# Kernel optimization log

Hardware: AMD Instinct MI355X
Metric: run time of the kernel (lower is better)

The kernel has to match this reference:

```python
import jax, jax.numpy as jnp
import numpy as np

NEG = -1e30


def setup_inputs() -> dict:
    key = jax.random.key(0)
    ks = jax.random.split(key, 8)
    B, d, Lc, Lq = 32, 128, 2048, 512
    C = jax.random.normal(ks[0], (B, d, Lc), dtype=jnp.float32)
    Q = jax.random.normal(ks[1], (B, d, Lq), dtype=jnp.float32)
    Cmask = jax.random.randint(ks[2], (B, Lc), 0, 2, dtype=jnp.int32)
    Qmask = jax.random.randint(ks[3], (B, Lq), 0, 2, dtype=jnp.int32)
    # xavier_uniform over (d, 1): bound = sqrt(6 / (d + 1))
    bnd = float(np.sqrt(6.0 / (d + 1)))
    w_c = jax.random.uniform(ks[4], (d, 1), minval=-bnd, maxval=bnd, dtype=jnp.float32)
    w_q = jax.random.uniform(ks[5], (d, 1), minval=-bnd, maxval=bnd, dtype=jnp.float32)
    bnd_m = float(np.sqrt(6.0 / (1 + d)))
    w_mul = jax.random.uniform(ks[6], (1, 1, d), minval=-bnd_m, maxval=bnd_m, dtype=jnp.float32)
    bias = jnp.zeros((1,), dtype=jnp.float32)
    return {"C": C, "Q": Q, "Cmask": Cmask, "Qmask": Qmask,
            "w_c": w_c, "w_q": w_q, "w_mul": w_mul, "bias": bias}


def reference(C, Q, Cmask, Qmask, w_c, w_q, w_mul, bias):
    # C: [B, d, Lc], Q: [B, d, Lq] -> transpose to token-major
    Ct = jnp.swapaxes(C, 1, 2)  # [B, Lc, d]
    Qt = jnp.swapaxes(Q, 1, 2)  # [B, Lq, d]
    cm = Cmask.astype(jnp.float32)[:, :, None]   # [B, Lc, 1]
    qm = Qmask.astype(jnp.float32)[:, None, :]   # [B, 1, Lq]
    # optimized trilinear similarity S: [B, Lc, Lq] (dropout p=0 / eval mode)
    s0 = Ct @ w_c                                  # [B, Lc, 1]
    s1 = jnp.swapaxes(Qt @ w_q, 1, 2)              # [B, 1, Lq]
    s2 = jnp.einsum('bcd,bqd->bcq', Ct * w_mul, Qt)  # [B, Lc, Lq]
    S = s0 + s1 + s2 + bias
    S1 = jax.nn.softmax(S + NEG * (1.0 - qm), axis=2)  # mask over query axis
    S2 = jax.nn.softmax(S + NEG * (1.0 - cm), axis=1)  # mask over context axis
    A = jnp.einsum('bcq,bqd->bcd', S1, Qt)             # [B, Lc, d]
    Bm = jnp.einsum('bck,bkd->bcd', jnp.einsum('bcq,bkq->bck', S1, S2), Ct)
    out = jnp.concatenate([Ct, A, Ct * A, Ct * Bm], axis=2)  # [B, Lc, 4d]
    return jnp.swapaxes(out, 1, 2)  # [B, 4d, Lc]
```

## Files before the change

kernel.cpp:

```cpp
#include <hip/hip_runtime.h>

#define B_ 32
#define D_ 128
#define LC 2048
#define LQ 512
#define CCH 16

#define NEGINF (-3.0e38f)

typedef __attribute__((ext_vector_type(8))) short bf16x8;
typedef __attribute__((ext_vector_type(4))) float f32x4;
typedef __attribute__((ext_vector_type(8))) unsigned short us8;
typedef __attribute__((ext_vector_type(8))) _Float16 f16x8;

__device__ __forceinline__ unsigned short bf16rne(float x) {
    unsigned int u = __float_as_uint(x);
    u = (u + 0x7FFFu + ((u >> 16) & 1u)) >> 16;
    return (unsigned short)u;
}

__device__ __forceinline__ void gll16(const void* g, void* l) {
    __builtin_amdgcn_global_load_lds((const __attribute__((address_space(1))) void*)g,
                                     (__attribute__((address_space(3))) void*)l, 16, 0, 0);
}

__global__ void k_dotw(const float* __restrict__ X, const float* __restrict__ w,
                       float* __restrict__ outv, int L) {
    int idx = blockIdx.x * 256 + threadIdx.x;
    int b = idx / L, x = idx - b * L;
    const float* Xp = X + (size_t)b * D_ * L + x;
    float acc = 0.f;
#pragma unroll 8
    for (int dd = 0; dd < D_; ++dd) acc += Xp[(size_t)dd * L] * w[dd];
    outv[idx] = acc;
}

__global__ void k_prep_C(const float* __restrict__ C, const float* __restrict__ wmul,
                         short* __restrict__ Ctw, short* __restrict__ Cb16) {
    int b = blockIdx.y, c0 = blockIdx.x * 64;
    __shared__ float Tf[128][65];
    __shared__ float wm[128];
    int t = threadIdx.x;
    if (t < 128) wm[t] = wmul[t];
    const float* Cb = C + (size_t)b * D_ * LC;
#pragma unroll
    for (int i = 0; i < 8; ++i) {
        int idx = t + i * 256;
        int d = idx >> 4, c4 = idx & 15;
        float4 v = *(const float4*)(Cb + (size_t)d * LC + c0 + c4 * 4);
        Tf[d][c4 * 4 + 0] = v.x; Tf[d][c4 * 4 + 1] = v.y;
        Tf[d][c4 * 4 + 2] = v.z; Tf[d][c4 * 4 + 3] = v.w;
        ushort4 cv;
        cv.x = bf16rne(v.x); cv.y = bf16rne(v.y); cv.z = bf16rne(v.z); cv.w = bf16rne(v.w);
        *(ushort4*)(Cb16 + ((size_t)b * D_ + d) * LC + c0 + c4 * 4) = cv;
    }
    __syncthreads();
    int c_l = t & 63, g = t >> 6;
    unsigned short u[32];
#pragma unroll
    for (int j = 0; j < 32; ++j) {
        int d = g * 32 + j;
        u[j] = bf16rne(Tf[d][c_l] * wm[d]);
    }
    short* dst = Ctw + ((size_t)b * LC + c0 + c_l) * D_ + g * 32;
#pragma unroll
    for (int k = 0; k < 4; ++k) *(us8*)(dst + k * 8) = *(const us8*)&u[k * 8];
}

__global__ void k_prep_Q(const float* __restrict__ Q, short* __restrict__ Qt16,
                         short* __restrict__ Wf) {
    int b = blockIdx.y, q0 = blockIdx.x * 64;
    __shared__ float Tf[128][65];
    int t = threadIdx.x;
    const float* Qb = Q + (size_t)b * D_ * LQ;
#pragma unroll
    for (int i = 0; i < 8; ++i) {
        int idx = t + i * 256;
        int d = idx >> 4, q4 = idx & 15;
        float4 v = *(const float4*)(Qb + (size_t)d * LQ + q0 + q4 * 4);
        Tf[d][q4 * 4 + 0] = v.x; Tf[d][q4 * 4 + 1] = v.y;
        Tf[d][q4 * 4 + 2] = v.z; Tf[d][q4 * 4 + 3] = v.w;
        ushort4 cv;
        cv.x = bf16rne(v.x); cv.y = bf16rne(v.y); cv.z = bf16rne(v.z); cv.w = bf16rne(v.w);
        *(ushort4*)(Wf + ((size_t)b * 256 + d) * LQ + q0 + q4 * 4) = cv;
    }
    __syncthreads();
    int q_l = t & 63, g = t >> 6;
    unsigned short u[32];
#pragma unroll
    for (int j = 0; j < 32; ++j) u[j] = bf16rne(Tf[g * 32 + j][q_l]);
    short* dst = Qt16 + ((size_t)b * LQ + q0 + q_l) * D_ + g * 32;
#pragma unroll
    for (int k = 0; k < 4; ++k) *(us8*)(dst + k * 8) = *(const us8*)&u[k * 8];
}

__global__ __launch_bounds__(256) void k_S_mfma(const short* __restrict__ Ctw,
                                                const short* __restrict__ Qt16,
                                                const float* __restrict__ s0,
                                                const float* __restrict__ s1,
                                                const float* __restrict__ bias,
                                                _Float16* __restrict__ S16) {
    int b = blockIdx.y;
    int cT = blockIdx.x >> 2, qT = blockIdx.x & 3;
    int c0 = cT * 128, q0 = qT * 128;
    int t = threadIdx.x, w = t >> 6, l = t & 63;
    int wm_ = w >> 1, wn = w & 1;
    __shared__ short As[128 * 64];
    __shared__ short Bs[128 * 64];
    f32x4 acc[4][4] = {};
    const short* Arow = Ctw + ((size_t)b * LC + c0) * D_;
    const short* Brow = Qt16 + ((size_t)b * LQ + q0) * D_;
    int lr = l >> 3, sl = l & 7;
    for (int kt = 0; kt < 2; ++kt) {
        __syncthreads();
#pragma unroll
        for (int i = 0; i < 4; ++i) {
            int r = w * 32 + i * 8 + lr;
            int g = sl ^ (r & 7);
            gll16(Arow + (size_t)r * D_ + kt * 64 + g * 8, &As[(w * 32 + i * 8) * 64]);
            gll16(Brow + (size_t)r * D_ + kt * 64 + g * 8, &Bs[(w * 32 + i * 8) * 64]);
        }
        __syncthreads();
#pragma unroll
        for (int ks = 0; ks < 2; ++ks) {
            int kg = ks * 4 + (l >> 4);
            bf16x8 af[4], bfr[4];
#pragma unroll
            for (int ms = 0; ms < 4; ++ms) {
                int m = wm_ * 64 + ms * 16 + (l & 15);
                af[ms] = *(const bf16x8*)&As[m * 64 + (kg ^ (m & 7)) * 8];
            }
#pragma unroll
            for (int ns = 0; ns < 4; ++ns) {
                int n = wn * 64 + ns * 16 + (l & 15);
                bfr[ns] = *(const bf16x8*)&Bs[n * 64 + (kg ^ (n & 7)) * 8];
            }
#pragma unroll
            for (int ms = 0; ms < 4; ++ms)
#pragma unroll
                for (int ns = 0; ns < 4; ++ns)
                    acc[ms][ns] = __builtin_amdgcn_mfma_f32_16x16x32_bf16(af[ms], bfr[ns], acc[ms][ns], 0, 0, 0);
        }
    }
    float bv = bias[0];
#pragma unroll
    for (int ms = 0; ms < 4; ++ms) {
        int cb = c0 + wm_ * 64 + ms * 16 + (l >> 4) * 4;
#pragma unroll
        for (int ns = 0; ns < 4; ++ns) {
            int q = q0 + wn * 64 + ns * 16 + (l & 15);
            float s1v = s1[b * LQ + q] + bv;
#pragma unroll
            for (int r = 0; r < 4; ++r) {
                int c = cb + r;
                S16[((size_t)b * LC + c) * LQ + q] = (_Float16)(acc[ms][ns][r] + s0[b * LC + c] + s1v);
            }
        }
    }
}

__global__ void k_rowsoftmax(_Float16* __restrict__ S16, const int* __restrict__ Qmask) {
    int row = blockIdx.x * 4 + (threadIdx.x >> 6);
    int lane = threadIdx.x & 63;
    int b = row / LC;
    _Float16* Sp = S16 + (size_t)row * LQ + lane * 8;
    f16x8 v = *(const f16x8*)Sp;
    const int* qm = Qmask + b * LQ + lane * 8;
    int4 m0 = *(const int4*)qm;
    int4 m1 = *(const int4*)(qm + 4);
    int mk[8] = {m0.x, m0.y, m0.z, m0.w, m1.x, m1.y, m1.z, m1.w};
    float vf[8];
#pragma unroll
    for (int k = 0; k < 8; ++k) vf[k] = (float)v[k];
    float mx = NEGINF;
#pragma unroll
    for (int k = 0; k < 8; ++k) if (mk[k]) mx = fmaxf(mx, vf[k]);
#pragma unroll
    for (int off = 32; off > 0; off >>= 1) mx = fmaxf(mx, __shfl_xor(mx, off, 64));
    float e[8];
    float s = 0.f;
#pragma unroll
    for (int k = 0; k < 8; ++k) { e[k] = __expf(vf[k] - mx); if (mk[k]) s += e[k]; }
#pragma unroll
    for (int off = 32; off > 0; off >>= 1) s += __shfl_xor(s, off, 64);
    float ri = 1.0f / s;
    unsigned short u[8];
#pragma unroll
    for (int k = 0; k < 8; ++k) u[k] = mk[k] ? bf16rne(e[k] * ri) : (unsigned short)0;
    *(us8*)Sp = *(const us8*)&u[0];
}

__global__ __launch_bounds__(256) void k_colstats_part(const _Float16* __restrict__ S16,
                                                       const int* __restrict__ Cmask,
                                                       float* __restrict__ pm,
                                                       float* __restrict__ pl) {
    int b = blockIdx.y;
    int q0 = blockIdx.x * 64;
    int ch = blockIdx.z;
    int t = threadIdx.x, ql = t & 63, cg = t >> 6;
    const int cbase = ch * (LC / CCH);
    const _Float16* Sb = S16 + (size_t)b * LC * LQ + (size_t)cbase * LQ + q0 + ql;
    const int* cm = Cmask + b * LC + cbase;
    float v[32];
#pragma unroll
    for (int i = 0; i < 32; ++i) {
        int c = cg + 4 * i;
        float x = (float)Sb[(size_t)c * LQ];
        v[i] = cm[c] ? x : NEGINF;
    }
    float m8[8];
#pragma unroll
    for (int j = 0; j < 8; ++j) m8[j] = v[j];
#pragma unroll
    for (int i = 8; i < 32; ++i) m8[i & 7] = fmaxf(m8[i & 7], v[i]);
    float m = fmaxf(fmaxf(fmaxf(m8[0], m8[1]), fmaxf(m8[2], m8[3])),
                    fmaxf(fmaxf(m8[4], m8[5]), fmaxf(m8[6], m8[7])));
    float s8[8];
#pragma unroll
    for (int j = 0; j < 8; ++j) s8[j] = 0.f;
#pragma unroll
    for (int i = 0; i < 32; ++i) s8[i & 7] += __expf(v[i] - m);
    float l = ((s8[0] + s8[1]) + (s8[2] + s8[3])) + ((s8[4] + s8[5]) + (s8[6] + s8[7]));
    if (m == NEGINF) l = 0.f;
    __shared__ float Ms[4][64], Ls[4][64];
    Ms[cg][ql] = m; Ls[cg][ql] = l;
    __syncthreads();
    if (t < 64) {
        float mm = Ms[0][ql], ll = Ls[0][ql];
#pragma unroll
        for (int g = 1; g < 4; ++g) {
            float m2 = Ms[g][ql], l2 = Ls[g][ql];
            float mn = fmaxf(mm, m2);
            ll = ll * __expf(mm - mn) + l2 * __expf(m2 - mn);
            mm = mn;
        }
        size_t o = ((size_t)ch * B_ + b) * LQ + q0 + ql;
        pm[o] = mm; pl[o] = ll;
    }
}

__global__ void k_colstats_comb(const float* __restrict__ pm, const float* __restrict__ pl,
                                float* __restrict__ colmax, float* __restrict__ colsum) {
    int idx = blockIdx.x * 256 + threadIdx.x;
    float m = NEGINF, l = 0.f;
#pragma unroll
    for (int ch = 0; ch < CCH; ++ch) {
        float m2 = pm[(size_t)ch * B_ * LQ + idx];
        float l2 = pl[(size_t)ch * B_ * LQ + idx];
        float mn = fmaxf(m, m2);
        l = l * __expf(m - mn) + l2 * __expf(m2 - mn);
        m = mn;
    }
    colmax[idx] = m; colsum[idx] = l;
}

__global__ __launch_bounds__(256) void k_V2_mfma(const short* __restrict__ Cb16,
                                                 const _Float16* __restrict__ S16,
                                                 const int* __restrict__ Cmask,
                                                 const float* __restrict__ colmax,
                                                 const float* __restrict__ colsum,
                                                 short* __restrict__ Wf) {
    int b = blockIdx.y;
    int q0 = blockIdx.x * 64;
    int t = threadIdx.x, w = t >> 6, l = t & 63;
    __shared__ short As[128 * 64];
    __shared__ short Bs[64 * 72];
    f32x4 acc[2][4] = {};
    const short* Arow = Cb16 + (size_t)b * D_ * LC;
    int lr = l >> 3, sl = l & 7;
    float cmx[16];
#pragma unroll
    for (int j2 = 0; j2 < 4; ++j2)
        *(float4*)&cmx[j2 * 4] = *(const float4*)(colmax + b * LQ + q0 + w * 16 + j2 * 4);
    const _Float16* Sq = S16 + (size_t)b * LC * LQ + q0 + w * 16;
    const int* cmb = Cmask + b * LC;

    for (int kt = 0; kt < 32; ++kt) {
        int ck = kt * 64;
        __syncthreads();
#pragma unroll
        for (int i = 0; i < 4; ++i) {
            int r = w * 32 + i * 8 + lr;
            int g = sl ^ (r & 7);
            gll16(Arow + (size_t)r * LC + ck + g * 8, &As[(w * 32 + i * 8) * 64]);
        }
        {
            float cmf = (float)cmb[ck + l];
            const _Float16* sp = Sq + (size_t)(ck + l) * LQ;
            f16x8 v0 = *(const f16x8*)sp;
            f16x8 v1 = *(const f16x8*)(sp + 8);
#pragma unroll
            for (int j = 0; j < 8; ++j)
                Bs[(w * 16 + j) * 72 + l] = (short)bf16rne(cmf * __expf((float)v0[j] - cmx[j]));
#pragma unroll
            for (int j = 0; j < 8; ++j)
                Bs[(w * 16 + 8 + j) * 72 + l] = (short)bf16rne(cmf * __expf((float)v1[j] - cmx[8 + j]));
        }
        __syncthreads();
#pragma unroll
        for (int ks = 0; ks < 2; ++ks) {
            int kg = ks * 4 + (l >> 4);
            bf16x8 af[2], bfr[4];
#pragma unroll
            for (int ms = 0; ms < 2; ++ms) {
                int m = w * 32 + ms * 16 + (l & 15);
                af[ms] = *(const bf16x8*)&As[m * 64 + (kg ^ (m & 7)) * 8];
            }
#pragma unroll
            for (int ns = 0; ns < 4; ++ns) {
                int n = ns * 16 + (l & 15);
                bfr[ns] = *(const bf16x8*)&Bs[n * 72 + kg * 8];
            }
#pragma unroll
            for (int ms = 0; ms < 2; ++ms)
#pragma unroll
                for (int ns = 0; ns < 4; ++ns)
                    acc[ms][ns] = __builtin_amdgcn_mfma_f32_16x16x32_bf16(af[ms], bfr[ns], acc[ms][ns], 0, 0, 0);
        }
    }
#pragma unroll
    for (int ms = 0; ms < 2; ++ms)
#pragma unroll
        for (int ns = 0; ns < 4; ++ns) {
            int q = q0 + ns * 16 + (l & 15);
            float csi = 1.0f / colsum[b * LQ + q];
#pragma unroll
            for (int r = 0; r < 4; ++r) {
                int dd = w * 32 + ms * 16 + (l >> 4) * 4 + r;
                Wf[((size_t)b * 256 + 128 + dd) * LQ + q] = (short)bf16rne(acc[ms][ns][r] * csi);
            }
        }
}

__global__ __launch_bounds__(512, 4) void k_out_mfma(const short* __restrict__ P1,
                                                     const short* __restrict__ Wf,
                                                     const float* __restrict__ C,
                                                     float* __restrict__ out) {
    int b = blockIdx.y;
    int c0 = blockIdx.x * 128;
    int t = threadIdx.x, w = t >> 6, l = t & 63;
    int wn = w & 3, wc = w >> 2;
    __shared__ short As[256 * 64];
    __shared__ short Bs[128 * 64];
    f32x4 acc[4][4] = {};
    const short* Arow = Wf + (size_t)b * 256 * LQ;
    const short* Brow = P1 + ((size_t)b * LC + c0) * LQ;
    int lr = l >> 3, sl = l & 7;
    for (int kt = 0; kt < 8; ++kt) {
        __syncthreads();
#pragma unroll
        for (int i = 0; i < 4; ++i) {
            int r = w * 32 + i * 8 + lr;
            int g = sl ^ lr;
            gll16(Arow + (size_t)r * LQ + kt * 64 + g * 8, &As[(w * 32 + i * 8) * 64]);
        }
#pragma unroll
        for (int i = 0; i < 2; ++i) {
            int r = w * 16 + i * 8 + lr;
            int g = sl ^ lr;
            gll16(Brow + (size_t)r * LQ + kt * 64 + g * 8, &Bs[(w * 16 + i * 8) * 64]);
        }
        __syncthreads();
#pragma unroll
        for (int ks = 0; ks < 2; ++ks) {
            int kg = ks * 4 + (l >> 4);
            bf16x8 af[4], bfr[4];
#pragma unroll
            for (int ms = 0; ms < 4; ++ms) {
                int m = wn * 64 + ms * 16 + (l & 15);
                af[ms] = *(const bf16x8*)&As[m * 64 + (kg ^ (m & 7)) * 8];
            }
#pragma unroll
            for (int ns = 0; ns < 4; ++ns) {
                int cc = wc * 64 + ns * 16 + (l & 15);
                bfr[ns] = *(const bf16x8*)&Bs[cc * 64 + (kg ^ (cc & 7)) * 8];
            }
#pragma unroll
            for (int ms = 0; ms < 4; ++ms)
#pragma unroll
                for (int ns = 0; ns < 4; ++ns)
                    acc[ms][ns] = __builtin_amdgcn_mfma_f32_16x16x32_bf16(af[ms], bfr[ns], acc[ms][ns], 0, 0, 0);
        }
    }
#pragma unroll
    for (int ms = 0; ms < 4; ++ms) {
        int nb = wn * 64 + ms * 16 + (l >> 4) * 4;
#pragma unroll
        for (int ns = 0; ns < 4; ++ns) {
            int c = c0 + wc * 64 + ns * 16 + (l & 15);
#pragma unroll
            for (int r = 0; r < 4; ++r) {
                int n = nb + r;
                float a = acc[ms][ns][r];
                if (n < 128) {
                    float cv = C[((size_t)b * D_ + n) * LC + c];
                    out[((size_t)b * 512 + n) * LC + c] = cv;
                    out[((size_t)b * 512 + 128 + n) * LC + c] = a;
                    out[((size_t)b * 512 + 256 + n) * LC + c] = cv * a;
                } else {
                    int dd = n - 128;
                    float cv = C[((size_t)b * D_ + dd) * LC + c];
                    out[((size_t)b * 512 + 384 + dd) * LC + c] = cv * a;
                }
            }
        }
    }
}

extern "C" void kernel_launch(void* const* d_in, const int* in_sizes, int n_in,
                              void* d_out, int out_size, void* d_ws, size_t ws_size,
                              hipStream_t stream) {
    const float* C     = (const float*)d_in[0];
    const float* Q     = (const float*)d_in[1];
    const int*   Cmask = (const int*)d_in[2];
    const int*   Qmask = (const int*)d_in[3];
    const float* w_c   = (const float*)d_in[4];
    const float* w_q   = (const float*)d_in[5];
    const float* w_mul = (const float*)d_in[6];
    const float* bias  = (const float*)d_in[7];
    float* out = (float*)d_out;

    _Float16* S16 = (_Float16*)d_ws;
    short* Cb16 = (short*)(S16 + (size_t)B_ * LC * LQ);
    short* Ctw  = Cb16 + (size_t)B_ * D_ * LC;
    short* Qt16 = Ctw + (size_t)B_ * LC * D_;
    short* Wf   = Qt16 + (size_t)B_ * LQ * D_;
    float* s0     = (float*)(Wf + (size_t)B_ * 256 * LQ);
    float* s1     = s0 + B_ * LC;
    float* colmax = s1 + B_ * LQ;
    float* colsum = colmax + B_ * LQ;
    float* pm     = colsum + B_ * LQ;
    float* pl     = pm + (size_t)CCH * B_ * LQ;

    hipLaunchKernelGGL(k_dotw, dim3(B_ * LC / 256), dim3(256), 0, stream, C, w_c, s0, LC);
    hipLaunchKernelGGL(k_dotw, dim3(B_ * LQ / 256), dim3(256), 0, stream, Q, w_q, s1, LQ);
    hipLaunchKernelGGL(k_prep_C, dim3(LC / 64, B_), dim3(256), 0, stream, C, w_mul, Ctw, Cb16);
    hipLaunchKernelGGL(k_prep_Q, dim3(LQ / 64, B_), dim3(256), 0, stream, Q, Qt16, Wf);
    hipLaunchKernelGGL(k_S_mfma, dim3((LC / 128) * (LQ / 128), B_), dim3(256), 0, stream,
                       Ctw, Qt16, s0, s1, bias, S16);
    hipLaunchKernelGGL(k_colstats_part, dim3(LQ / 64, B_, CCH), dim3(256), 0, stream,
                       S16, Cmask, pm, pl);
    hipLaunchKernelGGL(k_colstats_comb, dim3(B_ * LQ / 256), dim3(256), 0, stream,
                       pm, pl, colmax, colsum);
    hipLaunchKernelGGL(k_V2_mfma, dim3(LQ / 64, B_), dim3(256), 0, stream,
                       Cb16, S16, Cmask, colmax, colsum, Wf);
    hipLaunchKernelGGL(k_rowsoftmax, dim3(B_ * LC / 4), dim3(256), 0, stream, S16, Qmask);
    hipLaunchKernelGGL(k_out_mfma, dim3(LC / 128, B_), dim3(512), 0, stream,
                       (const short*)S16, Wf, C, out);
}
```

Baseline: 411.6 us.

## Fuse column softmax stats into S GEMM epilogue and double-buffer output GEMM

Partial column max and sum-exp statistics are now computed in the S GEMM epilogue from the fp16-rounded values and reduced across the 128-row tile through shared memory. This removes the separate colstats_part kernel and its full re-read of S16. Separately, the output GEMM gets double-buffered LDS staging with manual vmcnt waits, so the next K tile loads while the current one computes. That doubles its LDS use and drops the occupancy hint from launch bounds, which may cut occupancy.

Result: faster. 389.9 us (-5.3%).

```diff
diff --git a/kernel.cpp b/kernel.cpp
--- a/kernel.cpp
+++ b/kernel.cpp
@@ -99,7 +99,10 @@
                                                 const float* __restrict__ s0,
                                                 const float* __restrict__ s1,
                                                 const float* __restrict__ bias,
-                                                _Float16* __restrict__ S16) {
+                                                const int* __restrict__ Cmask,
+                                                _Float16* __restrict__ S16,
+                                                float* __restrict__ pm,
+                                                float* __restrict__ pl) {
     int b = blockIdx.y;
     int cT = blockIdx.x >> 2, qT = blockIdx.x & 3;
     int c0 = cT * 128, q0 = qT * 128;
@@ -143,19 +146,60 @@
         }
     }
     float bv = bias[0];
+    float s0v[16];
+    int cmv[16];
 #pragma unroll
     for (int ms = 0; ms < 4; ++ms) {
         int cb = c0 + wm_ * 64 + ms * 16 + (l >> 4) * 4;
-#pragma unroll
-        for (int ns = 0; ns < 4; ++ns) {
-            int q = q0 + wn * 64 + ns * 16 + (l & 15);
-            float s1v = s1[b * LQ + q] + bv;
+        float4 sv = *(const float4*)(s0 + b * LC + cb);
+        s0v[ms * 4 + 0] = sv.x; s0v[ms * 4 + 1] = sv.y;
+        s0v[ms * 4 + 2] = sv.z; s0v[ms * 4 + 3] = sv.w;
+        int4 cv = *(const int4*)(Cmask + b * LC + cb);
+        cmv[ms * 4 + 0] = cv.x; cmv[ms * 4 + 1] = cv.y;
+        cmv[ms * 4 + 2] = cv.z; cmv[ms * 4 + 3] = cv.w;
+    }
+    __syncthreads();
+    float* Mp = (float*)As;
+    float* Lp = (float*)Bs;
+    int prow = wm_ * 4 + (l >> 4);
+#pragma unroll
+    for (int ns = 0; ns < 4; ++ns) {
+        int qi = wn * 64 + ns * 16 + (l & 15);
+        int q = q0 + qi;
+        float s1v = s1[b * LQ + q] + bv;
+        float vq16[16];
+#pragma unroll
+        for (int ms = 0; ms < 4; ++ms) {
+            int cb = c0 + wm_ * 64 + ms * 16 + (l >> 4) * 4;
 #pragma unroll
             for (int r = 0; r < 4; ++r) {
-                int c = cb + r;
-                S16[((size_t)b * LC + c) * LQ + q] = (_Float16)(acc[ms][ns][r] + s0[b * LC + c] + s1v);
-            }
-        }
+                float vf = acc[ms][ns][r] + s0v[ms * 4 + r] + s1v;
+                _Float16 h = (_Float16)vf;
+                S16[((size_t)b * LC + cb + r) * LQ + q] = h;
+                vq16[ms * 4 + r] = (float)h;
+            }
+        }
+        float mt = NEGINF;
+#pragma unroll
+        for (int k = 0; k < 16; ++k) mt = fmaxf(mt, cmv[k] ? vq16[k] : NEGINF);
+        float st = 0.f;
+#pragma unroll
+        for (int k = 0; k < 16; ++k) st += cmv[k] ? __expf(vq16[k] - mt) : 0.f;
+        Mp[prow * 132 + qi] = mt;
+        Lp[prow * 132 + qi] = st;
+    }
+    __syncthreads();
+    if (t < 128) {
+        float mm = Mp[t], ll = Lp[t];
+#pragma unroll
+        for (int g = 1; g < 8; ++g) {
+            float m2 = Mp[g * 132 + t], l2 = Lp[g * 132 + t];
+            float mn = fmaxf(mm, m2);
+            ll = ll * __expf(mm - mn) + l2 * __expf(m2 - mn);
+            mm = mn;
+        }
+        size_t o = ((size_t)cT * B_ + b) * LQ + q0 + t;
+        pm[o] = mm; pl[o] = ll;
     }
 }
 
@@ -188,55 +232,6 @@
 #pragma unroll
     for (int k = 0; k < 8; ++k) u[k] = mk[k] ? bf16rne(e[k] * ri) : (unsigned short)0;
     *(us8*)Sp = *(const us8*)&u[0];
-}
-
-__global__ __launch_bounds__(256) void k_colstats_part(const _Float16* __restrict__ S16,
-                                                       const int* __restrict__ Cmask,
-                                                       float* __restrict__ pm,
-                                                       float* __restrict__ pl) {
-    int b = blockIdx.y;
-    int q0 = blockIdx.x * 64;
-    int ch = blockIdx.z;
-    int t = threadIdx.x, ql = t & 63, cg = t >> 6;
-    const int cbase = ch * (LC / CCH);
-    const _Float16* Sb = S16 + (size_t)b * LC * LQ + (size_t)cbase * LQ + q0 + ql;
-    const int* cm = Cmask + b * LC + cbase;
-    float v[32];
-#pragma unroll
-    for (int i = 0; i < 32; ++i) {
-        int c = cg + 4 * i;
-        float x = (float)Sb[(size_t)c * LQ];
-        v[i] = cm[c] ? x : NEGINF;
-    }
-    float m8[8];
-#pragma unroll
-    for (int j = 0; j < 8; ++j) m8[j] = v[j];
-#pragma unroll
-    for (int i = 8; i < 32; ++i) m8[i & 7] = fmaxf(m8[i & 7], v[i]);
-    float m = fmaxf(fmaxf(fmaxf(m8[0], m8[1]), fmaxf(m8[2], m8[3])),
-                    fmaxf(fmaxf(m8[4], m8[5]), fmaxf(m8[6], m8[7])));
-    float s8[8];
-#pragma unroll
-    for (int j = 0; j < 8; ++j) s8[j] = 0.f;
-#pragma unroll
-    for (int i = 0; i < 32; ++i) s8[i & 7] += __expf(v[i] - m);
-    float l = ((s8[0] + s8[1]) + (s8[2] + s8[3])) + ((s8[4] + s8[5]) + (s8[6] + s8[7]));
-    if (m == NEGINF) l = 0.f;
-    __shared__ float Ms[4][64], Ls[4][64];
-    Ms[cg][ql] = m; Ls[cg][ql] = l;
-    __syncthreads();
-    if (t < 64) {
-        float mm = Ms[0][ql], ll = Ls[0][ql];
-#pragma unroll
-        for (int g = 1; g < 4; ++g) {
-            float m2 = Ms[g][ql], l2 = Ls[g][ql];
-            float mn = fmaxf(mm, m2);
-            ll = ll * __expf(mm - mn) + l2 * __expf(m2 - mn);
-            mm = mn;
-        }
-        size_t o = ((size_t)ch * B_ + b) * LQ + q0 + ql;
-        pm[o] = mm; pl[o] = ll;
-    }
 }
 
 __global__ void k_colstats_comb(const float* __restrict__ pm, const float* __restrict__ pl,
@@ -332,35 +327,53 @@
         }
 }
 
-__global__ __launch_bounds__(512, 4) void k_out_mfma(const short* __restrict__ P1,
-                                                     const short* __restrict__ Wf,
-                                                     const float* __restrict__ C,
-                                                     float* __restrict__ out) {
+__global__ __launch_bounds__(512) void k_out_mfma(const short* __restrict__ P1,
+                                                  const short* __restrict__ Wf,
+                                                  const float* __restrict__ C,
+                                                  float* __restrict__ out) {
     int b = blockIdx.y;
     int c0 = blockIdx.x * 128;
     int t = threadIdx.x, w = t >> 6, l = t & 63;
     int wn = w & 3, wc = w >> 2;
-    __shared__ short As[256 * 64];
-    __shared__ short Bs[128 * 64];
+    __shared__ short As[2 * 256 * 64];
+    __shared__ short Bs[2 * 128 * 64];
     f32x4 acc[4][4] = {};
     const short* Arow = Wf + (size_t)b * 256 * LQ;
     const short* Brow = P1 + ((size_t)b * LC + c0) * LQ;
     int lr = l >> 3, sl = l & 7;
+    int g = sl ^ lr;
+
+#define STAGE(p, kt)                                                              \
+    {                                                                             \
+        short* Ad = As + (p) * (256 * 64);                                        \
+        short* Bd = Bs + (p) * (128 * 64);                                        \
+        _Pragma("unroll")                                                         \
+        for (int i = 0; i < 4; ++i) {                                             \
+            int r = w * 32 + i * 8 + lr;                                          \
+            gll16(Arow + (size_t)r * LQ + (kt) * 64 + g * 8,                      \
+                  &Ad[(w * 32 + i * 8) * 64]);                                    \
+        }                                                                         \
+        _Pragma("unroll")                                                         \
+        for (int i = 0; i < 2; ++i) {                                             \
+            int r = w * 16 + i * 8 + lr;                                          \
+            gll16(Brow + (size_t)r * LQ + (kt) * 64 + g * 8,                      \
+                  &Bd[(w * 16 + i * 8) * 64]);                                    \
+        }                                                                         \
+    }
+
+    STAGE(0, 0);
+    int cur = 0;
     for (int kt = 0; kt < 8; ++kt) {
-        __syncthreads();
-#pragma unroll
-        for (int i = 0; i < 4; ++i) {
-            int r = w * 32 + i * 8 + lr;
-            int g = sl ^ lr;
-            gll16(Arow + (size_t)r * LQ + kt * 64 + g * 8, &As[(w * 32 + i * 8) * 64]);
-        }
-#pragma unroll
-        for (int i = 0; i < 2; ++i) {
-            int r = w * 16 + i * 8 + lr;
-            int g = sl ^ lr;
-            gll16(Brow + (size_t)r * LQ + kt * 64 + g * 8, &Bs[(w * 16 + i * 8) * 64]);
-        }
-        __syncthreads();
+        if (kt < 7) {
+            STAGE(cur ^ 1, kt + 1);
+            asm volatile("s_waitcnt vmcnt(6)" ::: "memory");
+        } else {
+            asm volatile("s_waitcnt vmcnt(0)" ::: "memory");
+        }
+        __builtin_amdgcn_s_barrier();
+        __builtin_amdgcn_sched_barrier(0);
+        const short* Ac = As + cur * (256 * 64);
+        const short* Bc = Bs + cur * (128 * 64);
 #pragma unroll
         for (int ks = 0; ks < 2; ++ks) {
             int kg = ks * 4 + (l >> 4);
@@ -368,12 +381,12 @@
 #pragma unroll
             for (int ms = 0; ms < 4; ++ms) {
                 int m = wn * 64 + ms * 16 + (l & 15);
-                af[ms] = *(const bf16x8*)&As[m * 64 + (kg ^ (m & 7)) * 8];
+                af[ms] = *(const bf16x8*)&Ac[m * 64 + (kg ^ (m & 7)) * 8];
             }
 #pragma unroll
             for (int ns = 0; ns < 4; ++ns) {
                 int cc = wc * 64 + ns * 16 + (l & 15);
-                bfr[ns] = *(const bf16x8*)&Bs[cc * 64 + (kg ^ (cc & 7)) * 8];
+                bfr[ns] = *(const bf16x8*)&Bc[cc * 64 + (kg ^ (cc & 7)) * 8];
             }
 #pragma unroll
             for (int ms = 0; ms < 4; ++ms)
@@ -381,7 +394,10 @@
                 for (int ns = 0; ns < 4; ++ns)
                     acc[ms][ns] = __builtin_amdgcn_mfma_f32_16x16x32_bf16(af[ms], bfr[ns], acc[ms][ns], 0, 0, 0);
         }
-    }
+        __builtin_amdgcn_s_barrier();
+        cur ^= 1;
+    }
+#undef STAGE
 #pragma unroll
     for (int ms = 0; ms < 4; ++ms) {
         int nb = wn * 64 + ms * 16 + (l >> 4) * 4;
@@ -437,9 +453,7 @@
     hipLaunchKernelGGL(k_prep_C, dim3(LC / 64, B_), dim3(256), 0, stream, C, w_mul, Ctw, Cb16);
     hipLaunchKernelGGL(k_prep_Q, dim3(LQ / 64, B_), dim3(256), 0, stream, Q, Qt16, Wf);
     hipLaunchKernelGGL(k_S_mfma, dim3((LC / 128) * (LQ / 128), B_), dim3(256), 0, stream,
-                       Ctw, Qt16, s0, s1, bias, S16);
-    hipLaunchKernelGGL(k_colstats_part, dim3(LQ / 64, B_, CCH), dim3(256), 0, stream,
-                       S16, Cmask, pm, pl);
+                       Ctw, Qt16, s0, s1, bias, Cmask, S16, pm, pl);
     hipLaunchKernelGGL(k_colstats_comb, dim3(B_ * LQ / 256), dim3(256), 0, stream,
                        pm, pl, colmax, colsum);
     hipLaunchKernelGGL(k_V2_mfma, dim3(LQ / 64, B_), dim3(256), 0, stream,
```
